# Optimization experiments

Measured on AMD Instinct MI355X. Metric: run time of the kernel, lower is better.

Reference implementation:

```python
import jax, jax.numpy as jnp
import numpy as np

E = 64      # embedding_dim
H = 64      # h_dim
MLP = 1024  # mlp_dim (attention hidden)
PRE1 = 512  # mlp_pre_pool hidden
BNK = 1024  # bottleneck_dim
S = 256     # num scenes (equal-size groups replacing seq_start_end)
P = 16      # pedestrians per scene
B = S * P   # total batch of pedestrians
T = 8       # obs_len for vx/vy (only last row used)
EPS = 1e-5  # BatchNorm eps


def _bn(x, g, b, m, v):
    # eval-mode BatchNorm1d over the last (feature) axis
    return (x - m) * jax.lax.rsqrt(v + EPS) * g + b


def setup_inputs() -> dict:
    key = jax.random.key(0)
    ks = jax.random.split(key, 24)
    def n(k, shape, s=1.0):
        return jax.random.normal(k, shape, jnp.float32) * s
    return {
        "h_states": n(ks[0], (1, B, H)),
        "end_pos": n(ks[1], (B, 2)),
        "vx": n(ks[2], (T, B)),
        "vy": n(ks[3], (T, B)),
        "W_sp": n(ks[4], (2, E), 0.05), "b_sp": jnp.zeros((E,), jnp.float32),
        "W_vel": n(ks[5], (2, E), 0.05), "b_vel": jnp.zeros((E,), jnp.float32),
        "Wa1": n(ks[6], (2 * E, MLP), 0.05), "ba1": jnp.zeros((MLP,), jnp.float32),
        "ga1": jnp.ones((MLP,), jnp.float32), "bta1": jnp.zeros((MLP,), jnp.float32),
        "ma1": n(ks[7], (MLP,), 0.1), "va1": jax.random.uniform(ks[8], (MLP,), jnp.float32) + 0.5,
        "Wa2": n(ks[9], (MLP, 1), 0.05), "ba2": jnp.zeros((1,), jnp.float32),
        "ga2": jnp.ones((1,), jnp.float32), "bta2": jnp.zeros((1,), jnp.float32),
        "ma2": n(ks[10], (1,), 0.1), "va2": jax.random.uniform(ks[11], (1,), jnp.float32) + 0.5,
        "Wp1": n(ks[12], (E + H, PRE1), 0.05), "bp1": jnp.zeros((PRE1,), jnp.float32),
        "gp1": jnp.ones((PRE1,), jnp.float32), "btp1": jnp.zeros((PRE1,), jnp.float32),
        "mp1": n(ks[13], (PRE1,), 0.1), "vp1": jax.random.uniform(ks[14], (PRE1,), jnp.float32) + 0.5,
        "Wp2": n(ks[15], (PRE1, BNK), 0.05), "bp2": jnp.zeros((BNK,), jnp.float32),
        "gp2": jnp.ones((BNK,), jnp.float32), "btp2": jnp.zeros((BNK,), jnp.float32),
        "mp2": n(ks[16], (BNK,), 0.1), "vp2": jax.random.uniform(ks[17], (BNK,), jnp.float32) + 0.5,
        "num_scenes": S, "num_ped": P,
    }


def _forward(h_states, end_pos, vx, vy, W_sp, b_sp, W_vel, b_vel,
             Wa1, ba1, ga1, bta1, ma1, va1, Wa2, ba2, ga2, bta2, ma2, va2,
             Wp1, bp1, gp1, btp1, mp1, vp1, Wp2, bp2, gp2, btp2, mp2, vp2,
             num_scenes, num_ped):
    Sn, Pn = num_scenes, num_ped
    h = h_states.reshape(-1, H).reshape(Sn, Pn, H)          # per-scene hidden
    pos = end_pos.reshape(Sn, Pn, 2)
    # rel[s,i,j] = pos[s,j] - pos[s,i]  (repeat vs repeat_interleave in torch)
    rel = pos[:, None, :, :] - pos[:, :, None, :]
    rel_emb = rel @ W_sp + b_sp                              # [S,P,P,E]
    vel = jnp.stack([vx[-1], vy[-1]], axis=-1).reshape(Sn, Pn, 2)
    vel_emb = vel @ W_vel + b_vel                            # [S,P,E], indexed by row i
    vel_emb = jnp.broadcast_to(vel_emb[:, :, None, :], (Sn, Pn, Pn, E))
    att_in = jnp.concatenate([rel_emb, vel_emb], axis=-1)    # [S,P,P,2E]
    a = jax.nn.relu(_bn(att_in @ Wa1 + ba1, ga1, bta1, ma1, va1))
    scores = jax.nn.relu(_bn(a @ Wa2 + ba2, ga2, bta2, ma2, va2))  # [S,P,P,1]
    # torch.softmax(scores, dim=1) on an (N,1) tensor: softmax over the size-1
    # feature axis -> identically 1.0. Reproduced faithfully here.
    w = jax.nn.softmax(scores, axis=-1)
    h_rep = jnp.broadcast_to(h[:, None, :, :], (Sn, Pn, Pn, H))   # h[s,j] per (i,j)
    x = jnp.concatenate([rel_emb, h_rep], axis=-1) * (0.05 * w)   # [S,P,P,E+H]
    y = jax.nn.relu(_bn(x @ Wp1 + bp1, gp1, btp1, mp1, vp1))
    y = jax.nn.relu(_bn(y @ Wp2 + bp2, gp2, btp2, mp2, vp2))      # [S,P,P,BNK]
    pool = jnp.max(y, axis=2)                                     # max over neighbors j
    return pool.reshape(Sn * Pn, BNK)


def reference(h_states, end_pos, vx, vy, W_sp, b_sp, W_vel, b_vel,
              Wa1, ba1, ga1, bta1, ma1, va1, Wa2, ba2, ga2, bta2, ma2, va2,
              Wp1, bp1, gp1, btp1, mp1, vp1, Wp2, bp2, gp2, btp2, mp2, vp2,
              num_scenes, num_ped):
    return _forward(h_states, end_pos, vx, vy, W_sp, b_sp, W_vel, b_vel,
                    Wa1, ba1, ga1, bta1, ma1, va1, Wa2, ba2, ga2, bta2, ma2, va2,
                    Wp1, bp1, gp1, btp1, mp1, vp1, Wp2, bp2, gp2, btp2, mp2, vp2,
                    num_scenes, num_ped)
```

## Files before the change

kernel.cpp:

```cpp
#include <hip/hip_runtime.h>
#include <hip/hip_bf16.h>
#include <stdint.h>


typedef __bf16 bf16x8 __attribute__((ext_vector_type(8)));
typedef __bf16 bf16x2 __attribute__((ext_vector_type(2)));
typedef float  f32x4  __attribute__((ext_vector_type(4)));
typedef float  f32x2  __attribute__((ext_vector_type(2)));

#define BP2_OFF 0u
#define BP1_OFF 1048576u
#define MX_OFF  1114112u
#define MY_OFF  1116160u
#define CB_OFF  1118208u
#define SH_OFF  1120256u
#define A2_OFF  1122304u
#define C2_OFF  1126400u

#define Y1_LDS  0
#define HH_LDS  131072
#define LDS_SZ  147456

__device__ __forceinline__ unsigned short f2bf(float f) {
    union { float f; unsigned u; } c; c.f = f;
    unsigned u = c.u;
    return (unsigned short)((u + 0x7fffu + ((u >> 16) & 1u)) >> 16);
}
__device__ __forceinline__ float bfbits2f(unsigned hi) {
    union { unsigned u; float f; } c; c.u = hi; return c.f;
}
__device__ __forceinline__ unsigned pk_bf16(float a, float b) {
#if __has_builtin(__builtin_amdgcn_cvt_pk_bf16_f32)
    bf16x2 p = __builtin_amdgcn_cvt_pk_bf16_f32(a, b);
    union { bf16x2 v; unsigned u; } c; c.v = p; return c.u;
#else
    return (unsigned)f2bf(a) | ((unsigned)f2bf(b) << 16);
#endif
}
__device__ __forceinline__ int y1off(int r, int c16) {
    return r * 1024 + ((c16 ^ (r & 7)) << 4);
}

__global__ __launch_bounds__(256) void prep_pack_kernel(
    const float* __restrict__ Wsp,  const float* __restrict__ bsp,
    const float* __restrict__ Wp1,  const float* __restrict__ bp1,
    const float* __restrict__ gp1,  const float* __restrict__ btp1,
    const float* __restrict__ mp1,  const float* __restrict__ vp1,
    const float* __restrict__ Wp2,  const float* __restrict__ bp2,
    const float* __restrict__ gp2,  const float* __restrict__ btp2,
    const float* __restrict__ mp2,  const float* __restrict__ vp2,
    unsigned char* __restrict__ ws)
{
    __shared__ float tile[32 * 65];
    const int blk = blockIdx.x, t = threadIdx.x;

    if (blk < 272) {
        const float* src; int ncols, kb, ng;
        if (blk < 256) { kb = blk >> 4; ng = blk & 15; src = Wp2; ncols = 1024; }
        else { int b2 = blk - 256; kb = b2 >> 3; ng = b2 & 7; src = Wp1 + 64 * 512; ncols = 512; }
        const int k0 = kb * 32, n0 = ng * 64;
        #pragma unroll
        for (int it = 0; it < 2; ++it) {
            int c = t + it * 256;
            int r = c >> 4, c4 = c & 15;
            float4 v = *(const float4*)(src + (k0 + r) * ncols + n0 + c4 * 4);
            tile[r * 65 + c4 * 4 + 0] = v.x;
            tile[r * 65 + c4 * 4 + 1] = v.y;
            tile[r * 65 + c4 * 4 + 2] = v.z;
            tile[r * 65 + c4 * 4 + 3] = v.w;
        }
        __syncthreads();
        int ntl = t >> 6, l = t & 63;
        int nl = ntl * 16 + (l & 15), kl = (l >> 4) * 8;
        uint4 o;
        o.x = pk_bf16(tile[(kl + 0) * 65 + nl], tile[(kl + 1) * 65 + nl]);
        o.y = pk_bf16(tile[(kl + 2) * 65 + nl], tile[(kl + 3) * 65 + nl]);
        o.z = pk_bf16(tile[(kl + 4) * 65 + nl], tile[(kl + 5) * 65 + nl]);
        o.w = pk_bf16(tile[(kl + 6) * 65 + nl], tile[(kl + 7) * 65 + nl]);
        if (blk < 256) {
            ((uint4*)(ws + BP2_OFF))[(kb * 64 + ng * 4 + ntl) * 64 + l] = o;
        } else {
            ((uint4*)(ws + BP1_OFF))[((ng * 4 + ntl) * 2 + kb) * 64 + l] = o;
        }
    } else if (blk < 274) {
        int k = (blk - 272) * 256 + t;
        float a1 = gp1[k] * rsqrtf(vp1[k] + 1e-5f);
        float mx = 0.f, my = 0.f, cb = 0.f;
        for (int e = 0; e < 64; ++e) {
            float wv = Wp1[e * 512 + k];
            mx = fmaf(Wsp[e],      wv, mx);
            my = fmaf(Wsp[64 + e], wv, my);
            cb = fmaf(bsp[e],      wv, cb);
        }
        ((float*)(ws + MX_OFF))[k] = 0.05f * a1 * mx;
        ((float*)(ws + MY_OFF))[k] = 0.05f * a1 * my;
        ((float*)(ws + CB_OFF))[k] = 0.05f * a1 * cb + (bp1[k] - mp1[k]) * a1 + btp1[k];
        ((float*)(ws + SH_OFF))[k] = 0.05f * a1;
    } else {
        int n = (blk - 274) * 256 + t;
        float a = gp2[n] * rsqrtf(vp2[n] + 1e-5f);
        ((float*)(ws + A2_OFF))[n] = a;
        ((float*)(ws + C2_OFF))[n] = btp2[n] + (bp2[n] - mp2[n]) * a;
    }
}

__global__ __launch_bounds__(512, 2) void mm2_kernel(
    const float* __restrict__ hst,
    const float* __restrict__ epos,
    const unsigned char* __restrict__ ws,
    float* __restrict__ out)
{
    __shared__ __align__(16) unsigned char smem[LDS_SZ];

    const int s   = blockIdx.x >> 1;
    const int ih  = blockIdx.x & 1;
    const int tid = threadIdx.x;
    const int w    = tid >> 6;
    const int l    = tid & 63;
    const int quad = l >> 4;
    const int jl   = l & 15;

    {
        union { unsigned u[4]; bf16x8 v; } afh[2];
        #pragma unroll
        for (int kb = 0; kb < 2; ++kb) {
            const float4* hp = (const float4*)(hst + (s * 16 + jl) * 64 + kb * 32 + quad * 8);
            float4 v0 = hp[0], v1 = hp[1];
            afh[kb].u[0] = pk_bf16(v0.x, v0.y);
            afh[kb].u[1] = pk_bf16(v0.z, v0.w);
            afh[kb].u[2] = pk_bf16(v1.x, v1.y);
            afh[kb].u[3] = pk_bf16(v1.z, v1.w);
        }
        const f32x4 fz = {0.f, 0.f, 0.f, 0.f};
        f32x4 acch[4] = {fz, fz, fz, fz};
        #pragma unroll
        for (int kb = 0; kb < 2; ++kb) {
            #pragma unroll
            for (int ct = 0; ct < 4; ++ct) {
                bf16x8 bfr = *(const bf16x8*)(ws + BP1_OFF + ((((w * 4 + ct) * 2 + kb) * 64 + l) << 4));
                acch[ct] = __builtin_amdgcn_mfma_f32_16x16x32_bf16(afh[kb].v, bfr, acch[ct], 0, 0, 0);
            }
        }
        const float* SHg = (const float*)(ws + SH_OFF);
        const float* CBg = (const float*)(ws + CB_OFF);
        #pragma unroll
        for (int ct = 0; ct < 4; ++ct) {
            int col = (w * 4 + ct) * 16 + jl;
            float sh = SHg[col], cb = CBg[col];
            #pragma unroll
            for (int reg = 0; reg < 4; ++reg) {
                int j = quad * 4 + reg;
                float hv = fmaf(acch[ct][reg], sh, cb);
                *(unsigned short*)(smem + HH_LDS + j * 1024 + col * 2) = f2bf(hv);
            }
        }
    }
    __syncthreads();

    {
        const int i2 = tid >> 8;
        const int j  = (tid >> 4) & 15;
        const int kc = tid & 15;
        float rx[4], ry[4];
        float pjx = epos[s * 32 + j * 2], pjy = epos[s * 32 + j * 2 + 1];
        #pragma unroll
        for (int ii = 0; ii < 4; ++ii) {
            int ig_ = ih * 8 + i2 * 4 + ii;
            rx[ii] = pjx - epos[s * 32 + ig_ * 2];
            ry[ii] = pjy - epos[s * 32 + ig_ * 2 + 1];
        }
        const f32x2 zero2 = {0.f, 0.f};
        #pragma unroll
        for (int kk = 0; kk < 4; ++kk) {
            int k = kc * 32 + kk * 8;
            uint4 hh8 = *(const uint4*)(smem + HH_LDS + j * 1024 + k * 2);
            f32x4 mx0 = *(const f32x4*)(ws + MX_OFF + k * 4);
            f32x4 mx1 = *(const f32x4*)(ws + MX_OFF + k * 4 + 16);
            f32x4 my0 = *(const f32x4*)(ws + MY_OFF + k * 4);
            f32x4 my1 = *(const f32x4*)(ws + MY_OFF + k * 4 + 16);
            f32x2 mxp[4] = { {mx0[0],mx0[1]}, {mx0[2],mx0[3]}, {mx1[0],mx1[1]}, {mx1[2],mx1[3]} };
            f32x2 myp[4] = { {my0[0],my0[1]}, {my0[2],my0[3]}, {my1[0],my1[1]}, {my1[2],my1[3]} };
            f32x2 hhp[4];
            hhp[0][0] = bfbits2f(hh8.x << 16); hhp[0][1] = bfbits2f(hh8.x & 0xffff0000u);
            hhp[1][0] = bfbits2f(hh8.y << 16); hhp[1][1] = bfbits2f(hh8.y & 0xffff0000u);
            hhp[2][0] = bfbits2f(hh8.z << 16); hhp[2][1] = bfbits2f(hh8.z & 0xffff0000u);
            hhp[3][0] = bfbits2f(hh8.w << 16); hhp[3][1] = bfbits2f(hh8.w & 0xffff0000u);
            #pragma unroll
            for (int ii = 0; ii < 4; ++ii) {
                f32x2 rx2 = { rx[ii], rx[ii] };
                f32x2 ry2 = { ry[ii], ry[ii] };
                uint4 o;
                unsigned uu[4];
                #pragma unroll
                for (int p = 0; p < 4; ++p) {
                    f32x2 tt = __builtin_elementwise_fma(ry2, myp[p], hhp[p]);
                    tt = __builtin_elementwise_fma(rx2, mxp[p], tt);
                    tt = __builtin_elementwise_max(tt, zero2);
                    uu[p] = pk_bf16(tt[0], tt[1]);
                }
                o.x = uu[0]; o.y = uu[1]; o.z = uu[2]; o.w = uu[3];
                int r = (i2 * 4 + ii) * 16 + j;
                *(uint4*)(smem + Y1_LDS + y1off(r, kc * 4 + kk)) = o;
            }
        }
    }
    __syncthreads();

    const int ig = w & 1;
    const int ng = w >> 1;
    const float* A2 = (const float*)(ws + A2_OFF);
    const float* C2 = (const float*)(ws + C2_OFF);
    const f32x4 fzero = {0.f, 0.f, 0.f, 0.f};

    int ab[4];
    #pragma unroll
    for (int rt = 0; rt < 4; ++rt) {
        int r = (ig * 4 + rt) * 16 + jl;
        ab[rt] = Y1_LDS + r * 1024 + ((quad ^ (r & 7)) << 4);
    }

    #pragma unroll 1
    for (int chunk = 0; chunk < 2; ++chunk) {
        const int ntbase = ng * 16 + chunk * 8;
        const unsigned char* bp0 = ws + BP2_OFF + (ntbase << 10) + (l << 4);

        f32x4 acc[4][8];
        #pragma unroll
        for (int rt = 0; rt < 4; ++rt)
            #pragma unroll
            for (int ct = 0; ct < 8; ++ct) acc[rt][ct] = fzero;

        bf16x8 b0[8], b1[8];
        #pragma unroll
        for (int ct = 0; ct < 8; ++ct)
            b0[ct] = *(const bf16x8*)(bp0 + ct * 1024);

        #pragma unroll 1
        for (int t = 0; t < 8; ++t) {
            bf16x8 ae[4], ao[4];
            #pragma unroll
            for (int rt = 0; rt < 4; ++rt)
                ae[rt] = *(const bf16x8*)(smem + (ab[rt] + t * 128));
            #pragma unroll
            for (int ct = 0; ct < 8; ++ct)
                b1[ct] = *(const bf16x8*)(bp0 + (2 * t + 1) * 65536 + ct * 1024);
            #pragma unroll
            for (int rt = 0; rt < 4; ++rt)
                ao[rt] = *(const bf16x8*)(smem + ((ab[rt] + t * 128) ^ 64));
            #pragma unroll
            for (int rt = 0; rt < 4; ++rt)
                #pragma unroll
                for (int ct = 0; ct < 8; ++ct)
                    acc[rt][ct] = __builtin_amdgcn_mfma_f32_16x16x32_bf16(ae[rt], b0[ct], acc[rt][ct], 0, 0, 0);
            #pragma unroll
            for (int ct = 0; ct < 8; ++ct)
                b0[ct] = *(const bf16x8*)(bp0 + (2 * t + 2) * 65536 + ct * 1024);
            #pragma unroll
            for (int rt = 0; rt < 4; ++rt)
                #pragma unroll
                for (int ct = 0; ct < 8; ++ct)
                    acc[rt][ct] = __builtin_amdgcn_mfma_f32_16x16x32_bf16(ao[rt], b1[ct], acc[rt][ct], 0, 0, 0);
        }

        #pragma unroll
        for (int ct = 0; ct < 8; ++ct) {
            int col = (ntbase + ct) * 16 + jl;
            float a2 = A2[col], c2 = C2[col];
            #pragma unroll
            for (int rt = 0; rt < 4; ++rt) {
                float v0 = fmaxf(fmaf(acc[rt][ct][0], a2, c2), 0.f);
                float v1 = fmaxf(fmaf(acc[rt][ct][1], a2, c2), 0.f);
                float v2 = fmaxf(fmaf(acc[rt][ct][2], a2, c2), 0.f);
                float v3 = fmaxf(fmaf(acc[rt][ct][3], a2, c2), 0.f);
                float v = fmaxf(fmaxf(v0, v1), fmaxf(v2, v3));
                v = fmaxf(v, __shfl_xor(v, 16, 64));
                v = fmaxf(v, __shfl_xor(v, 32, 64));
                if (l < 16) {
                    int orow = s * 16 + ih * 8 + ig * 4 + rt;
                    __builtin_nontemporal_store(v, &out[orow * 1024 + col]);
                }
            }
        }
    }
}

extern "C" void kernel_launch(void* const* d_in, const int* in_sizes, int n_in,
                              void* d_out, int out_size, void* d_ws, size_t ws_size,
                              hipStream_t stream) {
    const float* hst  = (const float*)d_in[0];
    const float* epos = (const float*)d_in[1];
    const float* Wsp  = (const float*)d_in[4];
    const float* bsp  = (const float*)d_in[5];
    const float* Wp1  = (const float*)d_in[20];
    const float* bp1  = (const float*)d_in[21];
    const float* gp1  = (const float*)d_in[22];
    const float* btp1 = (const float*)d_in[23];
    const float* mp1  = (const float*)d_in[24];
    const float* vp1  = (const float*)d_in[25];
    const float* Wp2  = (const float*)d_in[26];
    const float* bp2  = (const float*)d_in[27];
    const float* gp2  = (const float*)d_in[28];
    const float* btp2 = (const float*)d_in[29];
    const float* mp2  = (const float*)d_in[30];
    const float* vp2  = (const float*)d_in[31];
    unsigned char* ws = (unsigned char*)d_ws;
    float* out = (float*)d_out;

    prep_pack_kernel<<<278, 256, 0, stream>>>(Wsp, bsp, Wp1, bp1, gp1, btp1, mp1, vp1,
                                              Wp2, bp2, gp2, btp2, mp2, vp2, ws);
    mm2_kernel<<<512, 512, 0, stream>>>(hst, epos, ws, out);
}
```

Baseline: 196.7 us.

## Switch second GEMM to 32x32x16 MFMA with repacked weight layout

Result: slower. 252.6 us (+28.4%).

```diff
diff --git a/kernel.cpp b/kernel.cpp
--- a/kernel.cpp
+++ b/kernel.cpp
@@ -7,6 +7,7 @@
 typedef __bf16 bf16x2 __attribute__((ext_vector_type(2)));
 typedef float  f32x4  __attribute__((ext_vector_type(4)));
 typedef float  f32x2  __attribute__((ext_vector_type(2)));
+typedef float  f32x16 __attribute__((ext_vector_type(16)));
 
 #define BP2_OFF 0u
 #define BP1_OFF 1048576u
@@ -19,7 +20,8 @@
 
 #define Y1_LDS  0
 #define HH_LDS  131072
-#define LDS_SZ  147456
+#define HH_STR  1040
+#define LDS_SZ  147712
 
 __device__ __forceinline__ unsigned short f2bf(float f) {
     union { float f; unsigned u; } c; c.f = f;
@@ -70,16 +72,25 @@
             tile[r * 65 + c4 * 4 + 3] = v.w;
         }
         __syncthreads();
-        int ntl = t >> 6, l = t & 63;
-        int nl = ntl * 16 + (l & 15), kl = (l >> 4) * 8;
-        uint4 o;
-        o.x = pk_bf16(tile[(kl + 0) * 65 + nl], tile[(kl + 1) * 65 + nl]);
-        o.y = pk_bf16(tile[(kl + 2) * 65 + nl], tile[(kl + 3) * 65 + nl]);
-        o.z = pk_bf16(tile[(kl + 4) * 65 + nl], tile[(kl + 5) * 65 + nl]);
-        o.w = pk_bf16(tile[(kl + 6) * 65 + nl], tile[(kl + 7) * 65 + nl]);
         if (blk < 256) {
-            ((uint4*)(ws + BP2_OFF))[(kb * 64 + ng * 4 + ntl) * 64 + l] = o;
+            int f = t >> 6, l = t & 63;
+            int kb16 = f >> 1, nt32 = f & 1;
+            int kr = kb16 * 16 + (l >> 5) * 8;
+            int nc = nt32 * 32 + (l & 31);
+            uint4 o;
+            o.x = pk_bf16(tile[(kr + 0) * 65 + nc], tile[(kr + 1) * 65 + nc]);
+            o.y = pk_bf16(tile[(kr + 2) * 65 + nc], tile[(kr + 3) * 65 + nc]);
+            o.z = pk_bf16(tile[(kr + 4) * 65 + nc], tile[(kr + 5) * 65 + nc]);
+            o.w = pk_bf16(tile[(kr + 6) * 65 + nc], tile[(kr + 7) * 65 + nc]);
+            ((uint4*)(ws + BP2_OFF))[((kb * 2 + kb16) * 32 + (ng * 2 + nt32)) * 64 + l] = o;
         } else {
+            int ntl = t >> 6, l = t & 63;
+            int nl = ntl * 16 + (l & 15), kl = (l >> 4) * 8;
+            uint4 o;
+            o.x = pk_bf16(tile[(kl + 0) * 65 + nl], tile[(kl + 1) * 65 + nl]);
+            o.y = pk_bf16(tile[(kl + 2) * 65 + nl], tile[(kl + 3) * 65 + nl]);
+            o.z = pk_bf16(tile[(kl + 4) * 65 + nl], tile[(kl + 5) * 65 + nl]);
+            o.w = pk_bf16(tile[(kl + 6) * 65 + nl], tile[(kl + 7) * 65 + nl]);
             ((uint4*)(ws + BP1_OFF))[((ng * 4 + ntl) * 2 + kb) * 64 + l] = o;
         }
     } else if (blk < 274) {
@@ -151,7 +162,7 @@
             for (int reg = 0; reg < 4; ++reg) {
                 int j = quad * 4 + reg;
                 float hv = fmaf(acch[ct][reg], sh, cb);
-                *(unsigned short*)(smem + HH_LDS + j * 1024 + col * 2) = f2bf(hv);
+                *(unsigned short*)(smem + HH_LDS + j * HH_STR + col * 2) = f2bf(hv);
             }
         }
     }
@@ -173,7 +184,7 @@
         #pragma unroll
         for (int kk = 0; kk < 4; ++kk) {
             int k = kc * 32 + kk * 8;
-            uint4 hh8 = *(const uint4*)(smem + HH_LDS + j * 1024 + k * 2);
+            uint4 hh8 = *(const uint4*)(smem + HH_LDS + j * HH_STR + k * 2);
             f32x4 mx0 = *(const f32x4*)(ws + MX_OFF + k * 4);
             f32x4 mx1 = *(const f32x4*)(ws + MX_OFF + k * 4 + 16);
             f32x4 my0 = *(const f32x4*)(ws + MY_OFF + k * 4);
@@ -206,77 +217,62 @@
     }
     __syncthreads();
 
-    const int ig = w & 1;
-    const int ng = w >> 1;
+    const int rt32 = w & 3;
+    const int nh   = w >> 2;
+    const int lm   = l & 31;
+    const int kh   = l >> 5;
+    const int r    = rt32 * 32 + lm;
+    const int rs   = r & 7;
+    const unsigned char* y1b = smem + Y1_LDS + r * 1024;
     const float* A2 = (const float*)(ws + A2_OFF);
     const float* C2 = (const float*)(ws + C2_OFF);
-    const f32x4 fzero = {0.f, 0.f, 0.f, 0.f};
-
-    int ab[4];
-    #pragma unroll
-    for (int rt = 0; rt < 4; ++rt) {
-        int r = (ig * 4 + rt) * 16 + jl;
-        ab[rt] = Y1_LDS + r * 1024 + ((quad ^ (r & 7)) << 4);
-    }
 
     #pragma unroll 1
     for (int chunk = 0; chunk < 2; ++chunk) {
-        const int ntbase = ng * 16 + chunk * 8;
-        const unsigned char* bp0 = ws + BP2_OFF + (ntbase << 10) + (l << 4);
-
-        f32x4 acc[4][8];
-        #pragma unroll
-        for (int rt = 0; rt < 4; ++rt)
-            #pragma unroll
-            for (int ct = 0; ct < 8; ++ct) acc[rt][ct] = fzero;
+        const int ntb = nh * 16 + chunk * 8;
+        const unsigned char* bp = ws + BP2_OFF + (ntb << 10) + (l << 4);
+
+        f32x16 acc[8];
+        #pragma unroll
+        for (int ct = 0; ct < 8; ++ct) acc[ct] = (f32x16){};
 
         bf16x8 b0[8], b1[8];
         #pragma unroll
         for (int ct = 0; ct < 8; ++ct)
-            b0[ct] = *(const bf16x8*)(bp0 + ct * 1024);
+            b0[ct] = *(const bf16x8*)(bp + ct * 1024);
 
         #pragma unroll 1
-        for (int t = 0; t < 8; ++t) {
-            bf16x8 ae[4], ao[4];
-            #pragma unroll
-            for (int rt = 0; rt < 4; ++rt)
-                ae[rt] = *(const bf16x8*)(smem + (ab[rt] + t * 128));
+        for (int t = 0; t < 16; ++t) {
+            int c16e = 4 * t + kh;
+            bf16x8 ae = *(const bf16x8*)(y1b + ((c16e ^ rs) << 4));
             #pragma unroll
             for (int ct = 0; ct < 8; ++ct)
-                b1[ct] = *(const bf16x8*)(bp0 + (2 * t + 1) * 65536 + ct * 1024);
-            #pragma unroll
-            for (int rt = 0; rt < 4; ++rt)
-                ao[rt] = *(const bf16x8*)(smem + ((ab[rt] + t * 128) ^ 64));
-            #pragma unroll
-            for (int rt = 0; rt < 4; ++rt)
+                b1[ct] = *(const bf16x8*)(bp + (2 * t + 1) * 32768 + ct * 1024);
+            bf16x8 ao = *(const bf16x8*)(y1b + (((c16e + 2) ^ rs) << 4));
+            #pragma unroll
+            for (int ct = 0; ct < 8; ++ct)
+                acc[ct] = __builtin_amdgcn_mfma_f32_32x32x16_bf16(ae, b0[ct], acc[ct], 0, 0, 0);
+            #pragma unroll
+            for (int ct = 0; ct < 8; ++ct)
+                b0[ct] = *(const bf16x8*)(bp + (2 * t + 2) * 32768 + ct * 1024);
+            #pragma unroll
+            for (int ct = 0; ct < 8; ++ct)
+                acc[ct] = __builtin_amdgcn_mfma_f32_32x32x16_bf16(ao, b1[ct], acc[ct], 0, 0, 0);
+        }
+
+        #pragma unroll
+        for (int ct = 0; ct < 8; ++ct) {
+            int col = (ntb + ct) * 32 + lm;
+            float a2 = A2[col], c2 = C2[col];
+            #pragma unroll
+            for (int i2 = 0; i2 < 2; ++i2) {
+                float v = fmaxf(fmaf(acc[ct][i2 * 8 + 0], a2, c2), 0.f);
                 #pragma unroll
-                for (int ct = 0; ct < 8; ++ct)
-                    acc[rt][ct] = __builtin_amdgcn_mfma_f32_16x16x32_bf16(ae[rt], b0[ct], acc[rt][ct], 0, 0, 0);
-            #pragma unroll
-            for (int ct = 0; ct < 8; ++ct)
-                b0[ct] = *(const bf16x8*)(bp0 + (2 * t + 2) * 65536 + ct * 1024);
-            #pragma unroll
-            for (int rt = 0; rt < 4; ++rt)
-                #pragma unroll
-                for (int ct = 0; ct < 8; ++ct)
-                    acc[rt][ct] = __builtin_amdgcn_mfma_f32_16x16x32_bf16(ao[rt], b1[ct], acc[rt][ct], 0, 0, 0);
-        }
-
-        #pragma unroll
-        for (int ct = 0; ct < 8; ++ct) {
-            int col = (ntbase + ct) * 16 + jl;
-            float a2 = A2[col], c2 = C2[col];
-            #pragma unroll
-            for (int rt = 0; rt < 4; ++rt) {
-                float v0 = fmaxf(fmaf(acc[rt][ct][0], a2, c2), 0.f);
-                float v1 = fmaxf(fmaf(acc[rt][ct][1], a2, c2), 0.f);
-                float v2 = fmaxf(fmaf(acc[rt][ct][2], a2, c2), 0.f);
-                float v3 = fmaxf(fmaf(acc[rt][ct][3], a2, c2), 0.f);
-                float v = fmaxf(fmaxf(v0, v1), fmaxf(v2, v3));
-                v = fmaxf(v, __shfl_xor(v, 16, 64));
+                for (int g = 1; g < 8; ++g)
+                    v = fmaxf(v, fmaxf(fmaf(acc[ct][i2 * 8 + g], a2, c2), 0.f));
                 v = fmaxf(v, __shfl_xor(v, 32, 64));
-                if (l < 16) {
-                    int orow = s * 16 + ih * 8 + ig * 4 + rt;
+                if (l < 32) {
+                    int orow = s * 16 + ih * 8 + rt32 * 2 + i2;
                     __builtin_nontemporal_store(v, &out[orow * 1024 + col]);
                 }
             }
```
